# Performance work log

Hardware: AMD Instinct MI355X
Metric: run time of the kernel (lower is better)

The kernel has to match this reference:

```python
import jax, jax.numpy as jnp
import numpy as np

N_HEAD = 16

def setup_inputs() -> dict:
    key = jax.random.key(0)
    ks = jax.random.split(key, 9)
    C = 1024
    s = 1.0 / np.sqrt(C)
    x = jax.random.normal(ks[0], (2, 2048, C), dtype=jnp.float32)
    Wq = jax.random.normal(ks[1], (C, C), dtype=jnp.float32) * s
    Wk = jax.random.normal(ks[2], (C, C), dtype=jnp.float32) * s
    Wv = jax.random.normal(ks[3], (C, C), dtype=jnp.float32) * s
    Wp = jax.random.normal(ks[4], (C, C), dtype=jnp.float32) * s
    z = jnp.zeros((C,), dtype=jnp.float32)
    return {"x": x, "Wq": Wq, "bq": z, "Wk": Wk, "bk": z, "Wv": Wv, "bv": z, "Wp": Wp, "bp": z}

def reference(x, Wq, bq, Wk, bk, Wv, bv, Wp, bp):
    B, T, C = x.shape
    H = N_HEAD
    D = C // H
    # QKV projections (Linear: x @ W.T + b), split heads -> [B, H, T, D]
    q = (x @ Wq.T + bq).reshape(B, T, H, D).transpose(0, 2, 1, 3)
    k = (x @ Wk.T + bk).reshape(B, T, H, D).transpose(0, 2, 1, 3)
    v = (x @ Wv.T + bv).reshape(B, T, H, D).transpose(0, 2, 1, 3)
    scale = 1.0 / jnp.sqrt(jnp.asarray(D, dtype=x.dtype))  # scaled_attn=True
    att = jnp.einsum('bhtd,bhsd->bhts', q, k) * scale      # [B,H,T,T]
    att = jax.nn.softmax(att, axis=-1)
    y = jnp.einsum('bhts,bhsd->bhtd', att, v)              # [B,H,T,D]
    y = y.transpose(0, 2, 1, 3).reshape(B, T, C)
    return y @ Wp.T + bp
```

## Files before the change

### kernel.cpp

```cpp
#include <hip/hip_runtime.h>
#include <stdint.h>

typedef unsigned short u16;
typedef __attribute__((ext_vector_type(8))) short short8;
typedef __attribute__((ext_vector_type(4))) float float4v;
typedef __attribute__((ext_vector_type(4))) u16 ushort4v;
typedef __attribute__((ext_vector_type(4))) unsigned int uint4v;

#define MFMA_BF16(a, b, c) __builtin_amdgcn_mfma_f32_16x16x32_bf16((a), (b), (c), 0, 0, 0)

__device__ __forceinline__ u16 f2bf(float f) {
    uint32_t u = __builtin_bit_cast(uint32_t, f);
    u += 0x7FFFu + ((u >> 16) & 1u);
    return (u16)(u >> 16);
}
__device__ __forceinline__ float bf2f(u16 b) {
    uint32_t u = ((uint32_t)b) << 16;
    return __builtin_bit_cast(float, u);
}
__device__ __forceinline__ void g2l16(const void* g, void* l) {
    __builtin_amdgcn_global_load_lds(
        (const __attribute__((address_space(1))) void*)g,
        (__attribute__((address_space(3))) void*)l, 16, 0, 0);
}

__global__ void cast_f32_bf16(const float* __restrict__ src, u16* __restrict__ dst, int n) {
    int i = (blockIdx.x * 256 + threadIdx.x) * 4;
    if (i < n) {
        float4v v = *(const float4v*)(src + i);
        ushort4v o;
        #pragma unroll
        for (int r = 0; r < 4; ++r) o[r] = f2bf(v[r]);
        *(ushort4v*)(dst + i) = o;
    }
}

__device__ __forceinline__ void gemm_core_128(const u16* __restrict__ A, const u16* __restrict__ B,
                                              int K, int m0, int n0, float4v acc[4][4]) {
    __shared__ u16 lA[128 * 64];
    __shared__ u16 lB[128 * 64];
    const int tid = threadIdx.x, lane = tid & 63;
    const int wave = tid >> 6, wm = wave >> 1, wn = wave & 1;
    const int l15 = lane & 15, quad = lane >> 4;

    for (int kt = 0; kt < K; kt += 64) {
        __syncthreads();
        #pragma unroll
        for (int i = 0; i < 4; ++i) {
            int f = i * 256 + tid;
            int row = f >> 3, kc = f & 7;
            g2l16(A + (size_t)(m0 + row) * K + kt + kc * 8, &lA[f * 8]);
            g2l16(B + (size_t)(n0 + row) * K + kt + kc * 8, &lB[f * 8]);
        }
        __syncthreads();
        #pragma unroll
        for (int ks = 0; ks < 2; ++ks) {
            short8 af[4], bf[4];
            #pragma unroll
            for (int t = 0; t < 4; ++t) {
                af[t] = *(const short8*)&lA[(wm * 64 + t * 16 + l15) * 64 + ks * 32 + quad * 8];
                bf[t] = *(const short8*)&lB[(wn * 64 + t * 16 + l15) * 64 + ks * 32 + quad * 8];
            }
            #pragma unroll
            for (int tm = 0; tm < 4; ++tm)
                #pragma unroll
                for (int tn = 0; tn < 4; ++tn)
                    acc[tm][tn] = MFMA_BF16(af[tm], bf[tn], acc[tm][tn]);
        }
    }
}

__global__ __launch_bounds__(256, 2) void gemm_qkv(
    const u16* __restrict__ xb, const u16* __restrict__ wqkv,
    const float* __restrict__ bq, const float* __restrict__ bk, const float* __restrict__ bv,
    u16* __restrict__ qo, u16* __restrict__ ko, u16* __restrict__ vto) {
    float4v acc[4][4] = {};
    gemm_core_128(xb, wqkv, 1024, blockIdx.y * 128, blockIdx.x * 128, acc);
    const int tid = threadIdx.x, lane = tid & 63;
    const int wave = tid >> 6, wm = wave >> 1, wn = wave & 1;
    const int l15 = lane & 15, quad = lane >> 4;
    const float QSC = 0.125f * 1.44269504088896340736f;
    #pragma unroll
    for (int tn = 0; tn < 4; ++tn) {
        int n = blockIdx.x * 128 + wn * 64 + tn * 16 + l15;
        int which = n >> 10, cb = n & 1023, h = cb >> 6, d = cb & 63;
        float bias = (which == 0) ? bq[cb] : ((which == 1) ? bk[cb] : bv[cb]);
        #pragma unroll
        for (int tm = 0; tm < 4; ++tm) {
            int mb = blockIdx.y * 128 + wm * 64 + tm * 16 + quad * 4;
            int b = mb >> 11, t0 = mb & 2047;
            if (which == 2) {
                ushort4v pk;
                #pragma unroll
                for (int r = 0; r < 4; ++r) pk[r] = f2bf(acc[tm][tn][r] + bias);
                *(ushort4v*)&vto[(((size_t)(b * 16 + h)) * 64 + d) * 2048 + t0] = pk;
            } else {
                #pragma unroll
                for (int r = 0; r < 4; ++r) {
                    float v = acc[tm][tn][r] + bias;
                    u16 bfv = f2bf(which == 0 ? v * QSC : v);
                    size_t addr = (((size_t)(b * 16 + h)) * 2048 + (t0 + r)) * 64 + d;
                    if (which == 0) qo[addr] = bfv; else ko[addr] = bfv;
                }
            }
        }
    }
}

__global__ __launch_bounds__(256, 2) void gemm_out(
    const u16* __restrict__ yb, const u16* __restrict__ wpb,
    const float* __restrict__ bp, float* __restrict__ out) {
    float4v acc[4][4] = {};
    gemm_core_128(yb, wpb, 1024, blockIdx.y * 128, blockIdx.x * 128, acc);
    const int tid = threadIdx.x, lane = tid & 63;
    const int wave = tid >> 6, wm = wave >> 1, wn = wave & 1;
    const int l15 = lane & 15, quad = lane >> 4;
    #pragma unroll
    for (int tn = 0; tn < 4; ++tn) {
        int n = blockIdx.x * 128 + wn * 64 + tn * 16 + l15;
        float bias = bp[n];
        #pragma unroll
        for (int tm = 0; tm < 4; ++tm) {
            #pragma unroll
            for (int r = 0; r < 4; ++r) {
                int m = blockIdx.y * 128 + wm * 64 + tm * 16 + quad * 4 + r;
                out[(size_t)m * 1024 + n] = acc[tm][tn][r] + bias;
            }
        }
    }
}

__global__ __launch_bounds__(256, 2) void attn(
    const u16* __restrict__ qg, const u16* __restrict__ kg,
    const u16* __restrict__ vtg, u16* __restrict__ yb) {
    __shared__ u16 kbuf[128 * 64];
    __shared__ u16 vtbuf[64 * 136];
    __shared__ u16 pbuf[128 * 136];
    __shared__ float lsum[2][128];

    const int tid = threadIdx.x, lane = tid & 63;
    const int wave = tid >> 6, wm = wave >> 1, wn = wave & 1;
    const int mh = wave & 1, nh = wave >> 1;
    const int l15 = lane & 15, quad = lane >> 4;
    const int bh = blockIdx.y, qt0 = blockIdx.x * 128;

    const u16* qbase = qg + (size_t)bh * 2048 * 64;
    const u16* kbase = kg + (size_t)bh * 2048 * 64;
    const u16* vtbase = vtg + (size_t)bh * 64 * 2048;

    short8 qf[4][2];
    #pragma unroll
    for (int tm = 0; tm < 4; ++tm)
        #pragma unroll
        for (int ks = 0; ks < 2; ++ks)
            qf[tm][ks] = *(const short8*)(qbase + (size_t)(qt0 + wm * 64 + tm * 16 + l15) * 64 + ks * 32 + quad * 8);

    float4v oacc[2][4] = {};
    float rs[4][4] = {};

    for (int it = 0; it < 16; ++it) {
        const int kv0 = it * 128;
        __syncthreads();
        #pragma unroll
        for (int i = 0; i < 4; ++i) {
            int f = i * 256 + tid, row = f >> 3, kc = f & 7;
            g2l16(kbase + (size_t)(kv0 + row) * 64 + kc * 8, &kbuf[f * 8]);
        }
        #pragma unroll
        for (int i = 0; i < 4; ++i) {
            int c = i * 256 + tid;
            int d = c >> 4, kvc = c & 15;
            uint4v val = *(const uint4v*)(vtbase + (size_t)d * 2048 + kv0 + kvc * 8);
            *(uint4v*)&vtbuf[d * 136 + kvc * 8] = val;
        }
        __syncthreads();
        float4v sacc[4][4] = {};
        #pragma unroll
        for (int ks = 0; ks < 2; ++ks) {
            short8 kf[4];
            #pragma unroll
            for (int tn = 0; tn < 4; ++tn)
                kf[tn] = *(const short8*)&kbuf[(wn * 64 + tn * 16 + l15) * 64 + ks * 32 + quad * 8];
            #pragma unroll
            for (int tm = 0; tm < 4; ++tm)
                #pragma unroll
                for (int tn = 0; tn < 4; ++tn)
                    sacc[tm][tn] = MFMA_BF16(qf[tm][ks], kf[tn], sacc[tm][tn]);
        }
        #pragma unroll
        for (int tm = 0; tm < 4; ++tm)
            #pragma unroll
            for (int tn = 0; tn < 4; ++tn)
                #pragma unroll
                for (int r = 0; r < 4; ++r) {
                    float p = __builtin_amdgcn_exp2f(sacc[tm][tn][r]);
                    u16 pb = f2bf(p);
                    rs[tm][r] += bf2f(pb);
                    pbuf[(wm * 64 + tm * 16 + quad * 4 + r) * 136 + wn * 64 + tn * 16 + l15] = pb;
                }
        __syncthreads();
        #pragma unroll
        for (int kst = 0; kst < 4; ++kst) {
            short8 afm[2], bfn[4];
            #pragma unroll
            for (int tmm = 0; tmm < 2; ++tmm)
                afm[tmm] = *(const short8*)&vtbuf[(mh * 32 + tmm * 16 + l15) * 136 + kst * 32 + quad * 8];
            #pragma unroll
            for (int tnn = 0; tnn < 4; ++tnn)
                bfn[tnn] = *(const short8*)&pbuf[(nh * 64 + tnn * 16 + l15) * 136 + kst * 32 + quad * 8];
            #pragma unroll
            for (int tmm = 0; tmm < 2; ++tmm)
                #pragma unroll
                for (int tnn = 0; tnn < 4; ++tnn)
                    oacc[tmm][tnn] = MFMA_BF16(afm[tmm], bfn[tnn], oacc[tmm][tnn]);
        }
    }
    #pragma unroll
    for (int tm = 0; tm < 4; ++tm)
        #pragma unroll
        for (int r = 0; r < 4; ++r) {
            float v = rs[tm][r];
            v += __shfl_xor(v, 1); v += __shfl_xor(v, 2);
            v += __shfl_xor(v, 4); v += __shfl_xor(v, 8);
            rs[tm][r] = v;
        }
    if (l15 == 0)
        #pragma unroll
        for (int tm = 0; tm < 4; ++tm)
            #pragma unroll
            for (int r = 0; r < 4; ++r)
                lsum[wn][wm * 64 + tm * 16 + quad * 4 + r] = rs[tm][r];
    __syncthreads();
    const int b = bh >> 4, h = bh & 15;
    #pragma unroll
    for (int tnn = 0; tnn < 4; ++tnn) {
        int qrow = nh * 64 + tnn * 16 + l15;
        float inv = 1.0f / (lsum[0][qrow] + lsum[1][qrow]);
        #pragma unroll
        for (int tmm = 0; tmm < 2; ++tmm) {
            int d0 = mh * 32 + tmm * 16 + quad * 4;
            ushort4v pk;
            #pragma unroll
            for (int r = 0; r < 4; ++r) pk[r] = f2bf(oacc[tmm][tnn][r] * inv);
            *(ushort4v*)&yb[((size_t)(b * 2048 + qt0 + qrow)) * 1024 + h * 64 + d0] = pk;
        }
    }
}

extern "C" void kernel_launch(void* const* d_in, const int* in_sizes, int n_in,
                              void* d_out, int out_size, void* d_ws, size_t ws_size,
                              hipStream_t stream) {
    const float* x  = (const float*)d_in[0];
    const float* Wq = (const float*)d_in[1];
    const float* bq = (const float*)d_in[2];
    const float* Wk = (const float*)d_in[3];
    const float* bk = (const float*)d_in[4];
    const float* Wv = (const float*)d_in[5];
    const float* bv = (const float*)d_in[6];
    const float* Wp = (const float*)d_in[7];
    const float* bp = (const float*)d_in[8];
    float* out = (float*)d_out;
    uint8_t* ws = (uint8_t*)d_ws;

    u16* xb   = (u16*)(ws);
    u16* wqkv = (u16*)(ws + (8u << 20));
    u16* wpb  = (u16*)(ws + (14u << 20));
    u16* qb   = (u16*)(ws + (16u << 20));
    u16* kb   = (u16*)(ws + (24u << 20));
    u16* vtb  = (u16*)(ws + (32u << 20));
    u16* yb   = (u16*)(ws + (40u << 20));

    cast_f32_bf16<<<4096, 256, 0, stream>>>(x,  xb,             4194304);
    cast_f32_bf16<<<1024, 256, 0, stream>>>(Wq, wqkv,           1048576);
    cast_f32_bf16<<<1024, 256, 0, stream>>>(Wk, wqkv + 1048576, 1048576);
    cast_f32_bf16<<<1024, 256, 0, stream>>>(Wv, wqkv + 2097152, 1048576);
    cast_f32_bf16<<<1024, 256, 0, stream>>>(Wp, wpb,            1048576);
    gemm_qkv<<<dim3(24, 32), 256, 0, stream>>>(xb, wqkv, bq, bk, bv, qb, kb, vtb);
    attn<<<dim3(16, 32), 256, 0, stream>>>(qb, kb, vtb, yb);
    gemm_out<<<dim3(8, 32), 256, 0, stream>>>(yb, wpb, bp, out);
}
```

Baseline: 221.1 us.

## Vectorize epilogue stores via transposed GEMMs, merge cast kernels, load V fragments directly

Merges the five cast launches into one kernel. The Q/K and output GEMMs swap their A/B operands so each lane holds four contiguous output columns, which allows vector bias loads and 8- or 16-byte stores in place of scattered scalar writes. In attention, S is computed transposed so P can be packed with perm into 8-byte LDS writes and row sums need only two shuffles. V fragments are now loaded straight from global memory into registers instead of staged through LDS. The trade-off is more live registers, plus per-lane global loads of V that are exposed within each iteration.

```diff
diff --git a/kernel.cpp b/kernel.cpp
--- a/kernel.cpp
+++ b/kernel.cpp
@@ -5,7 +5,7 @@
 typedef __attribute__((ext_vector_type(8))) short short8;
 typedef __attribute__((ext_vector_type(4))) float float4v;
 typedef __attribute__((ext_vector_type(4))) u16 ushort4v;
-typedef __attribute__((ext_vector_type(4))) unsigned int uint4v;
+typedef __attribute__((ext_vector_type(2))) unsigned int uint2v;
 
 #define MFMA_BF16(a, b, c) __builtin_amdgcn_mfma_f32_16x16x32_bf16((a), (b), (c), 0, 0, 0)
 
@@ -14,25 +14,29 @@
     u += 0x7FFFu + ((u >> 16) & 1u);
     return (u16)(u >> 16);
 }
-__device__ __forceinline__ float bf2f(u16 b) {
-    uint32_t u = ((uint32_t)b) << 16;
-    return __builtin_bit_cast(float, u);
-}
 __device__ __forceinline__ void g2l16(const void* g, void* l) {
     __builtin_amdgcn_global_load_lds(
         (const __attribute__((address_space(1))) void*)g,
         (__attribute__((address_space(3))) void*)l, 16, 0, 0);
 }
 
-__global__ void cast_f32_bf16(const float* __restrict__ src, u16* __restrict__ dst, int n) {
-    int i = (blockIdx.x * 256 + threadIdx.x) * 4;
-    if (i < n) {
-        float4v v = *(const float4v*)(src + i);
-        ushort4v o;
-        #pragma unroll
-        for (int r = 0; r < 4; ++r) o[r] = f2bf(v[r]);
-        *(ushort4v*)(dst + i) = o;
-    }
+__global__ void cast_all(const float* __restrict__ x, const float* __restrict__ wq,
+                         const float* __restrict__ wk, const float* __restrict__ wv,
+                         const float* __restrict__ wp,
+                         u16* __restrict__ xb, u16* __restrict__ wqkvb, u16* __restrict__ wpb) {
+    int bx = blockIdx.x;
+    const float* src; u16* dst; int base;
+    if (bx < 4096)      { src = x;  dst = xb;              base = bx; }
+    else if (bx < 5120) { src = wq; dst = wqkvb;           base = bx - 4096; }
+    else if (bx < 6144) { src = wk; dst = wqkvb + 1048576; base = bx - 5120; }
+    else if (bx < 7168) { src = wv; dst = wqkvb + 2097152; base = bx - 6144; }
+    else                { src = wp; dst = wpb;             base = bx - 7168; }
+    int i = base * 1024 + threadIdx.x * 4;
+    float4v v = *(const float4v*)(src + i);
+    ushort4v o;
+    #pragma unroll
+    for (int r = 0; r < 4; ++r) o[r] = f2bf(v[r]);
+    *(ushort4v*)(dst + i) = o;
 }
 
 __device__ __forceinline__ void gemm_core_128(const u16* __restrict__ A, const u16* __restrict__ B,
@@ -74,34 +78,52 @@
     const u16* __restrict__ xb, const u16* __restrict__ wqkv,
     const float* __restrict__ bq, const float* __restrict__ bk, const float* __restrict__ bv,
     u16* __restrict__ qo, u16* __restrict__ ko, u16* __restrict__ vto) {
-    float4v acc[4][4] = {};
-    gemm_core_128(xb, wqkv, 1024, blockIdx.y * 128, blockIdx.x * 128, acc);
+    const int bx = blockIdx.x, by = blockIdx.y;
     const int tid = threadIdx.x, lane = tid & 63;
     const int wave = tid >> 6, wm = wave >> 1, wn = wave & 1;
     const int l15 = lane & 15, quad = lane >> 4;
     const float QSC = 0.125f * 1.44269504088896340736f;
-    #pragma unroll
-    for (int tn = 0; tn < 4; ++tn) {
-        int n = blockIdx.x * 128 + wn * 64 + tn * 16 + l15;
-        int which = n >> 10, cb = n & 1023, h = cb >> 6, d = cb & 63;
-        float bias = (which == 0) ? bq[cb] : ((which == 1) ? bk[cb] : bv[cb]);
+
+    if (bx < 16) {
+        float4v acc[4][4] = {};
+        gemm_core_128(wqkv, xb, 1024, bx * 128, by * 128, acc);
+        const bool isq = bx < 8;
+        const float* bvec = isq ? bq : bk;
+        u16* dst = isq ? qo : ko;
         #pragma unroll
         for (int tm = 0; tm < 4; ++tm) {
-            int mb = blockIdx.y * 128 + wm * 64 + tm * 16 + quad * 4;
-            int b = mb >> 11, t0 = mb & 2047;
-            if (which == 2) {
+            int nloc = (bx & 7) * 128 + wm * 64 + tm * 16 + quad * 4;
+            int h = nloc >> 6, d0 = nloc & 63;
+            float4v bias = *(const float4v*)(bvec + nloc);
+            #pragma unroll
+            for (int tn = 0; tn < 4; ++tn) {
+                int t = by * 128 + wn * 64 + tn * 16 + l15;
+                int b = t >> 11, tt = t & 2047;
+                ushort4v pk;
+                #pragma unroll
+                for (int r = 0; r < 4; ++r) {
+                    float v = acc[tm][tn][r] + bias[r];
+                    pk[r] = f2bf(isq ? v * QSC : v);
+                }
+                *(ushort4v*)&dst[(((size_t)(b * 16 + h)) * 2048 + tt) * 64 + d0] = pk;
+            }
+        }
+    } else {
+        float4v acc[4][4] = {};
+        gemm_core_128(xb, wqkv, 1024, by * 128, bx * 128, acc);
+        #pragma unroll
+        for (int tn = 0; tn < 4; ++tn) {
+            int n = bx * 128 + wn * 64 + tn * 16 + l15;
+            int cb = n & 1023, h = cb >> 6, d = cb & 63;
+            float bias = bv[cb];
+            #pragma unroll
+            for (int tm = 0; tm < 4; ++tm) {
+                int mb = by * 128 + wm * 64 + tm * 16 + quad * 4;
+                int b = mb >> 11, t0 = mb & 2047;
                 ushort4v pk;
                 #pragma unroll
                 for (int r = 0; r < 4; ++r) pk[r] = f2bf(acc[tm][tn][r] + bias);
                 *(ushort4v*)&vto[(((size_t)(b * 16 + h)) * 64 + d) * 2048 + t0] = pk;
-            } else {
-                #pragma unroll
-                for (int r = 0; r < 4; ++r) {
-                    float v = acc[tm][tn][r] + bias;
-                    u16 bfv = f2bf(which == 0 ? v * QSC : v);
-                    size_t addr = (((size_t)(b * 16 + h)) * 2048 + (t0 + r)) * 64 + d;
-                    if (which == 0) qo[addr] = bfv; else ko[addr] = bfv;
-                }
             }
         }
     }
@@ -111,21 +133,21 @@
     const u16* __restrict__ yb, const u16* __restrict__ wpb,
     const float* __restrict__ bp, float* __restrict__ out) {
     float4v acc[4][4] = {};
-    gemm_core_128(yb, wpb, 1024, blockIdx.y * 128, blockIdx.x * 128, acc);
+    gemm_core_128(wpb, yb, 1024, blockIdx.x * 128, blockIdx.y * 128, acc);
     const int tid = threadIdx.x, lane = tid & 63;
     const int wave = tid >> 6, wm = wave >> 1, wn = wave & 1;
     const int l15 = lane & 15, quad = lane >> 4;
     #pragma unroll
-    for (int tn = 0; tn < 4; ++tn) {
-        int n = blockIdx.x * 128 + wn * 64 + tn * 16 + l15;
-        float bias = bp[n];
-        #pragma unroll
-        for (int tm = 0; tm < 4; ++tm) {
-            #pragma unroll
-            for (int r = 0; r < 4; ++r) {
-                int m = blockIdx.y * 128 + wm * 64 + tm * 16 + quad * 4 + r;
-                out[(size_t)m * 1024 + n] = acc[tm][tn][r] + bias;
-            }
+    for (int tm = 0; tm < 4; ++tm) {
+        int n = blockIdx.x * 128 + wm * 64 + tm * 16 + quad * 4;
+        float4v bias = *(const float4v*)(bp + n);
+        #pragma unroll
+        for (int tn = 0; tn < 4; ++tn) {
+            int t = blockIdx.y * 128 + wn * 64 + tn * 16 + l15;
+            float4v o;
+            #pragma unroll
+            for (int r = 0; r < 4; ++r) o[r] = acc[tm][tn][r] + bias[r];
+            *(float4v*)&out[(size_t)t * 1024 + n] = o;
         }
     }
 }
@@ -134,12 +156,12 @@
     const u16* __restrict__ qg, const u16* __restrict__ kg,
     const u16* __restrict__ vtg, u16* __restrict__ yb) {
     __shared__ u16 kbuf[128 * 64];
-    __shared__ u16 vtbuf[64 * 136];
     __shared__ u16 pbuf[128 * 136];
     __shared__ float lsum[2][128];
 
     const int tid = threadIdx.x, lane = tid & 63;
-    const int wave = tid >> 6, wm = wave >> 1, wn = wave & 1;
+    const int wave = tid >> 6;
+    const int sm = wave >> 1, sn = wave & 1;
     const int mh = wave & 1, nh = wave >> 1;
     const int l15 = lane & 15, quad = lane >> 4;
     const int bh = blockIdx.y, qt0 = blockIdx.x * 128;
@@ -150,13 +172,13 @@
 
     short8 qf[4][2];
     #pragma unroll
-    for (int tm = 0; tm < 4; ++tm)
+    for (int tn = 0; tn < 4; ++tn)
         #pragma unroll
         for (int ks = 0; ks < 2; ++ks)
-            qf[tm][ks] = *(const short8*)(qbase + (size_t)(qt0 + wm * 64 + tm * 16 + l15) * 64 + ks * 32 + quad * 8);
+            qf[tn][ks] = *(const short8*)(qbase + (size_t)(qt0 + sn * 64 + tn * 16 + l15) * 64 + ks * 32 + quad * 8);
 
     float4v oacc[2][4] = {};
-    float rs[4][4] = {};
+    float rs[4] = {};
 
     for (int it = 0; it < 16; ++it) {
         const int kv0 = it * 128;
@@ -166,45 +188,46 @@
             int f = i * 256 + tid, row = f >> 3, kc = f & 7;
             g2l16(kbase + (size_t)(kv0 + row) * 64 + kc * 8, &kbuf[f * 8]);
         }
-        #pragma unroll
-        for (int i = 0; i < 4; ++i) {
-            int c = i * 256 + tid;
-            int d = c >> 4, kvc = c & 15;
-            uint4v val = *(const uint4v*)(vtbase + (size_t)d * 2048 + kv0 + kvc * 8);
-            *(uint4v*)&vtbuf[d * 136 + kvc * 8] = val;
-        }
+        short8 vf[4][2];
+        #pragma unroll
+        for (int kst = 0; kst < 4; ++kst)
+            #pragma unroll
+            for (int tmm = 0; tmm < 2; ++tmm)
+                vf[kst][tmm] = *(const short8*)(vtbase + (size_t)(mh * 32 + tmm * 16 + l15) * 2048 + kv0 + kst * 32 + quad * 8);
         __syncthreads();
         float4v sacc[4][4] = {};
         #pragma unroll
         for (int ks = 0; ks < 2; ++ks) {
             short8 kf[4];
             #pragma unroll
-            for (int tn = 0; tn < 4; ++tn)
-                kf[tn] = *(const short8*)&kbuf[(wn * 64 + tn * 16 + l15) * 64 + ks * 32 + quad * 8];
-            #pragma unroll
             for (int tm = 0; tm < 4; ++tm)
+                kf[tm] = *(const short8*)&kbuf[(sm * 64 + tm * 16 + l15) * 64 + ks * 32 + quad * 8];
+            #pragma unroll
+            for (int tm = 0; tm < 4; ++tm)
                 #pragma unroll
                 for (int tn = 0; tn < 4; ++tn)
-                    sacc[tm][tn] = MFMA_BF16(qf[tm][ks], kf[tn], sacc[tm][tn]);
+                    sacc[tm][tn] = MFMA_BF16(kf[tm], qf[tn][ks], sacc[tm][tn]);
         }
         #pragma unroll
         for (int tm = 0; tm < 4; ++tm)
             #pragma unroll
-            for (int tn = 0; tn < 4; ++tn)
+            for (int tn = 0; tn < 4; ++tn) {
+                uint32_t u[4];
                 #pragma unroll
                 for (int r = 0; r < 4; ++r) {
                     float p = __builtin_amdgcn_exp2f(sacc[tm][tn][r]);
-                    u16 pb = f2bf(p);
-                    rs[tm][r] += bf2f(pb);
-                    pbuf[(wm * 64 + tm * 16 + quad * 4 + r) * 136 + wn * 64 + tn * 16 + l15] = pb;
+                    u[r] = __builtin_bit_cast(uint32_t, p);
+                    rs[tn] += __builtin_bit_cast(float, u[r] & 0xFFFF0000u);
                 }
+                uint2v pk;
+                pk.x = __builtin_amdgcn_perm(u[1], u[0], 0x07060302u);
+                pk.y = __builtin_amdgcn_perm(u[3], u[2], 0x07060302u);
+                *(uint2v*)&pbuf[(sn * 64 + tn * 16 + l15) * 136 + sm * 64 + tm * 16 + quad * 4] = pk;
+            }
         __syncthreads();
         #pragma unroll
         for (int kst = 0; kst < 4; ++kst) {
-            short8 afm[2], bfn[4];
-            #pragma unroll
-            for (int tmm = 0; tmm < 2; ++tmm)
-                afm[tmm] = *(const short8*)&vtbuf[(mh * 32 + tmm * 16 + l15) * 136 + kst * 32 + quad * 8];
+            short8 bfn[4];
             #pragma unroll
             for (int tnn = 0; tnn < 4; ++tnn)
                 bfn[tnn] = *(const short8*)&pbuf[(nh * 64 + tnn * 16 + l15) * 136 + kst * 32 + quad * 8];
@@ -212,24 +235,20 @@
             for (int tmm = 0; tmm < 2; ++tmm)
                 #pragma unroll
                 for (int tnn = 0; tnn < 4; ++tnn)
-                    oacc[tmm][tnn] = MFMA_BF16(afm[tmm], bfn[tnn], oacc[tmm][tnn]);
-        }
-    }
-    #pragma unroll
-    for (int tm = 0; tm < 4; ++tm)
-        #pragma unroll
-        for (int r = 0; r < 4; ++r) {
-            float v = rs[tm][r];
-            v += __shfl_xor(v, 1); v += __shfl_xor(v, 2);
-            v += __shfl_xor(v, 4); v += __shfl_xor(v, 8);
-            rs[tm][r] = v;
-        }
-    if (l15 == 0)
-        #pragma unroll
-        for (int tm = 0; tm < 4; ++tm)
-            #pragma unroll
-            for (int r = 0; r < 4; ++r)
-                lsum[wn][wm * 64 + tm * 16 + quad * 4 + r] = rs[tm][r];
+                    oacc[tmm][tnn] = MFMA_BF16(vf[kst][tmm], bfn[tnn], oacc[tmm][tnn]);
+        }
+    }
+    #pragma unroll
+    for (int tn = 0; tn < 4; ++tn) {
+        float v = rs[tn];
+        v += __shfl_xor(v, 16);
+        v += __shfl_xor(v, 32);
+        rs[tn] = v;
+    }
+    if (lane < 16)
+        #pragma unroll
+        for (int tn = 0; tn < 4; ++tn)
+            lsum[sm][sn * 64 + tn * 16 + l15] = rs[tn];
     __syncthreads();
     const int b = bh >> 4, h = bh & 15;
     #pragma unroll
@@ -270,11 +289,7 @@
     u16* vtb  = (u16*)(ws + (32u << 20));
     u16* yb   = (u16*)(ws + (40u << 20));
 
-    cast_f32_bf16<<<4096, 256, 0, stream>>>(x,  xb,             4194304);
-    cast_f32_bf16<<<1024, 256, 0, stream>>>(Wq, wqkv,           1048576);
-    cast_f32_bf16<<<1024, 256, 0, stream>>>(Wk, wqkv + 1048576, 1048576);
-    cast_f32_bf16<<<1024, 256, 0, stream>>>(Wv, wqkv + 2097152, 1048576);
-    cast_f32_bf16<<<1024, 256, 0, stream>>>(Wp, wpb,            1048576);
+    cast_all<<<8192, 256, 0, stream>>>(x, Wq, Wk, Wv, Wp, xb, wqkv, wpb);
     gemm_qkv<<<dim3(24, 32), 256, 0, stream>>>(xb, wqkv, bq, bk, bv, qb, kb, vtb);
     attn<<<dim3(16, 32), 256, 0, stream>>>(qb, kb, vtb, yb);
     gemm_out<<<dim3(8, 32), 256, 0, stream>>>(yb, wpb, bp, out);
```

Result: faster. 209.6 us (-5.2%).
